# Kernel optimization log

Hardware: AMD Instinct MI355X
Metric: run time of the kernel (lower is better)

Reference implementation:

```python
import jax, jax.numpy as jnp
import numpy as np

B = 8192
L = 2  # number of clipped photonic layers


def _pauli_z_matrix():
    # Z expectation per wire for each of the 16 basis states; wire 0 = MSB.
    k = np.arange(16)
    Z = np.stack([1 - 2 * ((k >> 3) & 1),
                  1 - 2 * ((k >> 2) & 1),
                  1 - 2 * ((k >> 1) & 1),
                  1 - 2 * (k & 1)], axis=1).astype(np.float32)
    return jnp.asarray(Z)  # (16, 4)


def setup_inputs() -> dict:
    key = jax.random.key(0)
    ks = jax.random.split(key, 14)
    x = jax.random.normal(ks[0], (B, 1, 28, 28), dtype=jnp.float32)
    # input photonic layer (no clip)
    w_in = 0.5 * jax.random.normal(ks[1], (2, 2), dtype=jnp.float32)
    b_in = 0.1 * jax.random.normal(ks[2], (2,), dtype=jnp.float32)
    scale_in = 1.0 + 0.1 * jax.random.normal(ks[3], (2,), dtype=jnp.float32)
    shift_in = 0.05 * jax.random.normal(ks[4], (2,), dtype=jnp.float32)
    # L clipped photonic layers (clip applied at construction in torch)
    Wc = jnp.clip(0.5 * jax.random.normal(ks[5], (L, 2, 2), dtype=jnp.float32), -5.0, 5.0)
    bc = jnp.clip(0.1 * jax.random.normal(ks[6], (L, 2), dtype=jnp.float32), -5.0, 5.0)
    scalec = 1.0 + 0.1 * jax.random.normal(ks[7], (L, 2), dtype=jnp.float32)
    shiftc = 0.05 * jax.random.normal(ks[8], (L, 2), dtype=jnp.float32)
    # final linear of classical branch: Linear(2, 1)
    w_out = 0.5 * jax.random.normal(ks[9], (1, 2), dtype=jnp.float32)
    b_out = 0.1 * jax.random.normal(ks[10], (1,), dtype=jnp.float32)
    # fixed random 16x16 unitary standing in for tq.RandomLayer(n_ops=8, 4 wires)
    rng = np.random.default_rng(0)
    A = rng.normal(size=(16, 16)) + 1j * rng.normal(size=(16, 16))
    Q, _ = np.linalg.qr(A)
    U_re = jnp.asarray(Q.real.astype(np.float32))
    U_im = jnp.asarray(Q.imag.astype(np.float32))
    # classifier Linear(785, 1)  (original declares 786 but combined feat is 785)
    w_cls = 0.03 * jax.random.normal(ks[11], (1, 785), dtype=jnp.float32)
    b_cls = 0.1 * jax.random.normal(ks[12], (1,), dtype=jnp.float32)
    return {"x": x, "w_in": w_in, "b_in": b_in, "scale_in": scale_in,
            "shift_in": shift_in, "Wc": Wc, "bc": bc, "scalec": scalec,
            "shiftc": shiftc, "w_out": w_out, "b_out": b_out,
            "U_re": U_re, "U_im": U_im, "w_cls": w_cls, "b_cls": b_cls}


def reference(x, w_in, b_in, scale_in, shift_in, Wc, bc, scalec, shiftc,
              w_out, b_out, U_re, U_im, w_cls, b_cls):
    bsz = x.shape[0]
    # ---- classical branch: mean/std features through photonic-style MLP ----
    mean = jnp.mean(x, axis=(1, 2, 3))[:, None]
    std = jnp.std(x, axis=(1, 2, 3), ddof=1)[:, None]  # torch unbiased std
    h = jnp.concatenate([mean, std], axis=1)  # (B, 2)
    h = jnp.tanh(h @ w_in.T + b_in) * scale_in + shift_in
    for i in range(Wc.shape[0]):
        h = jnp.tanh(h @ Wc[i].T + bc[i]) * scalec[i] + shiftc[i]
    cls_out = h @ w_out.T + b_out  # (B, 1)
    # ---- quantum branch: all 196 2x2 patches batched in one pass ----
    img = x.reshape(bsz, 28, 28)
    # (B,14,2,14,2) -> (B,14,14,2,2) -> (B,196,4) with patch pixel order
    # [x[r,c], x[r,c+1], x[r+1,c], x[r+1,c+1]] matching the torch loop.
    p = img.reshape(bsz, 14, 2, 14, 2).transpose(0, 1, 3, 2, 4).reshape(bsz, 196, 4)
    half = 0.5 * p
    a = jnp.stack([jnp.cos(half), jnp.sin(half)], axis=-1)  # (B,196,4,2) RY|0> amps
    # product state over 4 qubits -> (B,196,16)
    psi = jnp.einsum('bpi,bpj,bpk,bpl->bpijkl',
                     a[:, :, 0], a[:, :, 1], a[:, :, 2], a[:, :, 3]
                     ).reshape(bsz, 196, 16)
    re = psi @ U_re.T
    im = psi @ U_im.T
    probs = re * re + im * im  # (B,196,16)
    Z = _pauli_z_matrix()
    qfeat = (probs @ Z).reshape(bsz, 196 * 4)  # (B, 784)
    # ---- fuse + classify ----
    combined = jnp.concatenate([cls_out, qfeat], axis=1)  # (B, 785)
    logits = combined @ w_cls.T + b_cls
    return jax.nn.sigmoid(logits)
```

## Files before the change

kernel.cpp:

```cpp
#include <hip/hip_runtime.h>
#include <hip/hip_bf16.h>
#include <math.h>


#define NPATCH 196
#define NIMG   8192
#define ROWB   80

typedef __bf16 bf16x8 __attribute__((ext_vector_type(8)));
typedef float  f32x4  __attribute__((ext_vector_type(4)));

union Frag { bf16x8 v; uint4 u; unsigned us[4]; };

static __device__ inline unsigned short bfbits(float f) {
    __hip_bfloat16 h = __float2bfloat16(f);
    unsigned short s; __builtin_memcpy(&s, &h, 2); return s;
}
static __device__ inline unsigned packbf(float lo, float hi) {
    return (unsigned)bfbits(lo) | ((unsigned)bfbits(hi) << 16);
}

__global__ __launch_bounds__(256) void fraud_kernel(
    const float* __restrict__ x,
    const float* __restrict__ w_in,
    const float* __restrict__ b_in,
    const float* __restrict__ scale_in,
    const float* __restrict__ shift_in,
    const float* __restrict__ Wc,
    const float* __restrict__ bc,
    const float* __restrict__ scalec,
    const float* __restrict__ shiftc,
    const float* __restrict__ w_out,
    const float* __restrict__ b_out,
    const float* __restrict__ U_re,
    const float* __restrict__ U_im,
    const float* __restrict__ w_cls,
    const float* __restrict__ b_cls,
    float* __restrict__ out)
{
    __shared__ __align__(16) unsigned char lds[256 * ROWB];
    __shared__ __align__(16) float wlds[784];
    __shared__ float red[3][4];

    const int tid  = threadIdx.x;
    const int lane = tid & 63;
    const int wv   = tid >> 6;
    const int n16  = lane & 15;
    const int q    = lane >> 4;
    const int img  = blockIdx.x;

    for (int i = tid; i < 784; i += 256) wlds[i] = w_cls[1 + i];

    Frag bre, bim;
    bre.u = make_uint4(0u, 0u, 0u, 0u);
    bim.u = make_uint4(0u, 0u, 0u, 0u);
    if (q < 2) {
        const float* pr = U_re + n16 * 16 + q * 8;
        const float* pi = U_im + n16 * 16 + q * 8;
        bre.us[0] = packbf(pr[0], pr[1]); bre.us[1] = packbf(pr[2], pr[3]);
        bre.us[2] = packbf(pr[4], pr[5]); bre.us[3] = packbf(pr[6], pr[7]);
        bim.us[0] = packbf(pi[0], pi[1]); bim.us[1] = packbf(pi[2], pi[3]);
        bim.us[2] = packbf(pi[4], pi[5]); bim.us[3] = packbf(pi[6], pi[7]);
    }

    const float* xp = x + (size_t)img * 784;
    float sum = 0.f, sumsq = 0.f;
    uint4 lo = make_uint4(0u, 0u, 0u, 0u);
    uint4 hi = make_uint4(0u, 0u, 0u, 0u);
    if (tid < NPATCH) {
        const int rr = tid / 14;
        const int cc = tid - rr * 14;
        const float2 top = *(const float2*)(xp + (2 * rr) * 28 + 2 * cc);
        const float2 bot = *(const float2*)(xp + (2 * rr + 1) * 28 + 2 * cc);
        const float x0 = top.x, x1 = top.y, x2 = bot.x, x3 = bot.y;

        sum   = x0 + x1 + x2 + x3;
        sumsq = x0 * x0 + x1 * x1 + x2 * x2 + x3 * x3;

        float s0, c0, s1, c1, s2, c2, s3, c3;
        __sincosf(0.5f * x0, &s0, &c0);
        __sincosf(0.5f * x1, &s1, &c1);
        __sincosf(0.5f * x2, &s2, &c2);
        __sincosf(0.5f * x3, &s3, &c3);

        const float a01[4] = { c0 * c1, c0 * s1, s0 * c1, s0 * s1 };
        const float a23[4] = { c2 * c3, c2 * s3, s2 * c3, s2 * s3 };

        lo.x = packbf(a01[0] * a23[0], a01[0] * a23[1]);
        lo.y = packbf(a01[0] * a23[2], a01[0] * a23[3]);
        lo.z = packbf(a01[1] * a23[0], a01[1] * a23[1]);
        lo.w = packbf(a01[1] * a23[2], a01[1] * a23[3]);
        hi.x = packbf(a01[2] * a23[0], a01[2] * a23[1]);
        hi.y = packbf(a01[2] * a23[2], a01[2] * a23[3]);
        hi.z = packbf(a01[3] * a23[0], a01[3] * a23[1]);
        hi.w = packbf(a01[3] * a23[2], a01[3] * a23[3]);
    }
    unsigned* row = (unsigned*)(lds + tid * ROWB);
    *(uint4*)(row)      = lo;
    *(uint4*)(row + 4)  = hi;
    *(uint4*)(row + 8)  = make_uint4(0u, 0u, 0u, 0u);
    *(uint4*)(row + 12) = make_uint4(0u, 0u, 0u, 0u);
    __syncthreads();

    const float sg0 = (n16 & 8) ? -1.f : 1.f;
    const float sg1 = (n16 & 4) ? -1.f : 1.f;
    const float sg2 = (n16 & 2) ? -1.f : 1.f;
    const float sg3 = (n16 & 1) ? -1.f : 1.f;

    float qacc = 0.f;
    const unsigned char* wb = lds + wv * 64 * ROWB;

    auto do_tile = [&](int t) {
        Frag a;
        a.u = *(const uint4*)(wb + (t * 16 + n16) * ROWB + q * 16);
        f32x4 cr = {0.f, 0.f, 0.f, 0.f}, ci = {0.f, 0.f, 0.f, 0.f};
        cr = __builtin_amdgcn_mfma_f32_16x16x32_bf16(a.v, bre.v, cr, 0, 0, 0);
        ci = __builtin_amdgcn_mfma_f32_16x16x32_bf16(a.v, bim.v, ci, 0, 0, 0);
        #pragma unroll
        for (int j = 0; j < 4; ++j) {
            const int m = wv * 64 + t * 16 + q * 4 + j;
            float zc = 0.f;
            if (m < NPATCH) {
                const float4 wq = *(const float4*)(wlds + 4 * m);
                zc = wq.x * sg0 + wq.y * sg1 + wq.z * sg2 + wq.w * sg3;
            }
            const float prob = cr[j] * cr[j] + ci[j] * ci[j];
            qacc = fmaf(prob, zc, qacc);
        }
    };
    if (wv < 3) {
        do_tile(0); do_tile(1); do_tile(2); do_tile(3);
    } else {
        do_tile(0);
    }

    #pragma unroll
    for (int off = 1; off < 64; off <<= 1) {
        sum   += __shfl_xor(sum,   off, 64);
        sumsq += __shfl_xor(sumsq, off, 64);
        qacc  += __shfl_xor(qacc,  off, 64);
    }
    if (lane == 0) {
        red[0][wv] = sum;
        red[1][wv] = sumsq;
        red[2][wv] = qacc;
    }
    __syncthreads();

    if (tid == 0) {
        const float S  = red[0][0] + red[0][1] + red[0][2] + red[0][3];
        const float SS = red[1][0] + red[1][1] + red[1][2] + red[1][3];
        const float QS = red[2][0] + red[2][1] + red[2][2] + red[2][3];

        const float mean = S * (1.f / 784.f);
        float var = (SS - S * S * (1.f / 784.f)) * (1.f / 783.f);
        var = fmaxf(var, 0.f);
        const float stdv = sqrtf(var);

        float h0 = mean, h1 = stdv;
        {
            const float t0 = tanhf(h0 * w_in[0] + h1 * w_in[1] + b_in[0]);
            const float t1 = tanhf(h0 * w_in[2] + h1 * w_in[3] + b_in[1]);
            h0 = t0 * scale_in[0] + shift_in[0];
            h1 = t1 * scale_in[1] + shift_in[1];
        }
        #pragma unroll
        for (int l = 0; l < 2; ++l) {
            const float t0 = tanhf(h0 * Wc[l * 4 + 0] + h1 * Wc[l * 4 + 1] + bc[l * 2 + 0]);
            const float t1 = tanhf(h0 * Wc[l * 4 + 2] + h1 * Wc[l * 4 + 3] + bc[l * 2 + 1]);
            h0 = t0 * scalec[l * 2 + 0] + shiftc[l * 2 + 0];
            h1 = t1 * scalec[l * 2 + 1] + shiftc[l * 2 + 1];
        }
        const float cls   = h0 * w_out[0] + h1 * w_out[1] + b_out[0];
        const float logit = b_cls[0] + w_cls[0] * cls + QS;
        out[img] = 1.f / (1.f + __expf(-logit));
    }
}

extern "C" void kernel_launch(void* const* d_in, const int* in_sizes, int n_in,
                              void* d_out, int out_size, void* d_ws, size_t ws_size,
                              hipStream_t stream) {
    const float* x        = (const float*)d_in[0];
    const float* w_in     = (const float*)d_in[1];
    const float* b_in     = (const float*)d_in[2];
    const float* scale_in = (const float*)d_in[3];
    const float* shift_in = (const float*)d_in[4];
    const float* Wc       = (const float*)d_in[5];
    const float* bc       = (const float*)d_in[6];
    const float* scalec   = (const float*)d_in[7];
    const float* shiftc   = (const float*)d_in[8];
    const float* w_out    = (const float*)d_in[9];
    const float* b_out    = (const float*)d_in[10];
    const float* U_re     = (const float*)d_in[11];
    const float* U_im     = (const float*)d_in[12];
    const float* w_cls    = (const float*)d_in[13];
    const float* b_cls    = (const float*)d_in[14];
    float* out = (float*)d_out;

    fraud_kernel<<<NIMG, 256, 0, stream>>>(x, w_in, b_in, scale_in, shift_in,
                                           Wc, bc, scalec, shiftc, w_out, b_out,
                                           U_re, U_im, w_cls, b_cls, out);
}
```

Baseline: 115.7 us.

## Process 16 images per block with per-wave image loop and precomputed Z weights

```diff
diff --git a/kernel.cpp b/kernel.cpp
--- a/kernel.cpp
+++ b/kernel.cpp
@@ -5,6 +5,8 @@
 
 #define NPATCH 196
 #define NIMG   8192
+#define GIMG   16
+#define NBLK   (NIMG / GIMG)
 #define ROWB   80
 
 typedef __bf16 bf16x8 __attribute__((ext_vector_type(8)));
@@ -18,6 +20,25 @@
 }
 static __device__ inline unsigned packbf(float lo, float hi) {
     return (unsigned)bfbits(lo) | ((unsigned)bfbits(hi) << 16);
+}
+
+static __device__ inline void psi_pack(float x0, float x1, float x2, float x3,
+                                       uint4& lo, uint4& hi) {
+    float s0, c0, s1, c1, s2, c2, s3, c3;
+    __sincosf(0.5f * x0, &s0, &c0);
+    __sincosf(0.5f * x1, &s1, &c1);
+    __sincosf(0.5f * x2, &s2, &c2);
+    __sincosf(0.5f * x3, &s3, &c3);
+    const float a01[4] = { c0 * c1, c0 * s1, s0 * c1, s0 * s1 };
+    const float a23[4] = { c2 * c3, c2 * s3, s2 * c3, s2 * s3 };
+    lo.x = packbf(a01[0] * a23[0], a01[0] * a23[1]);
+    lo.y = packbf(a01[0] * a23[2], a01[0] * a23[3]);
+    lo.z = packbf(a01[1] * a23[0], a01[1] * a23[1]);
+    lo.w = packbf(a01[1] * a23[2], a01[1] * a23[3]);
+    hi.x = packbf(a01[2] * a23[0], a01[2] * a23[1]);
+    hi.y = packbf(a01[2] * a23[2], a01[2] * a23[3]);
+    hi.z = packbf(a01[3] * a23[0], a01[3] * a23[1]);
+    hi.w = packbf(a01[3] * a23[2], a01[3] * a23[3]);
 }
 
 __global__ __launch_bounds__(256) void fraud_kernel(
@@ -39,17 +60,23 @@
     float* __restrict__ out)
 {
     __shared__ __align__(16) unsigned char lds[256 * ROWB];
-    __shared__ __align__(16) float wlds[784];
-    __shared__ float red[3][4];
+    __shared__ float zc[NPATCH * 17];
+    __shared__ float accS[GIMG], accV[GIMG], accQ[GIMG];
 
     const int tid  = threadIdx.x;
     const int lane = tid & 63;
     const int wv   = tid >> 6;
     const int n16  = lane & 15;
     const int q    = lane >> 4;
-    const int img  = blockIdx.x;
-
-    for (int i = tid; i < 784; i += 256) wlds[i] = w_cls[1 + i];
+    const int img0 = blockIdx.x * GIMG;
+
+    for (int i = tid; i < NPATCH * 16; i += 256) {
+        const int m = i >> 4, n = i & 15;
+        const float* wp = w_cls + 1 + 4 * m;
+        const float w0 = wp[0], w1 = wp[1], w2 = wp[2], w3 = wp[3];
+        zc[m * 17 + n] = ((n & 8) ? -w0 : w0) + ((n & 4) ? -w1 : w1)
+                       + ((n & 2) ? -w2 : w2) + ((n & 1) ? -w3 : w3);
+    }
 
     Frag bre, bim;
     bre.u = make_uint4(0u, 0u, 0u, 0u);
@@ -63,94 +90,130 @@
         bim.us[2] = packbf(pi[4], pi[5]); bim.us[3] = packbf(pi[6], pi[7]);
     }
 
-    const float* xp = x + (size_t)img * 784;
-    float sum = 0.f, sumsq = 0.f;
-    uint4 lo = make_uint4(0u, 0u, 0u, 0u);
-    uint4 hi = make_uint4(0u, 0u, 0u, 0u);
-    if (tid < NPATCH) {
-        const int rr = tid / 14;
-        const int cc = tid - rr * 14;
+    unsigned char* wbase = lds + wv * 64 * ROWB;
+    unsigned* myrow = (unsigned*)(wbase + lane * ROWB);
+    *(uint4*)(myrow + 8)  = make_uint4(0u, 0u, 0u, 0u);
+    *(uint4*)(myrow + 12) = make_uint4(0u, 0u, 0u, 0u);
+
+    __syncthreads();
+
+    const int imgw0 = img0 + wv * 4;
+
+    float2 ctop, cbot;
+    {
+        const int p = lane, rr = p / 14, cc = p - rr * 14;
+        const float* xp = x + (size_t)imgw0 * 784;
+        ctop = *(const float2*)(xp + (2 * rr) * 28 + 2 * cc);
+        cbot = *(const float2*)(xp + (2 * rr + 1) * 28 + 2 * cc);
+    }
+
+    float rS = 0.f, rV = 0.f, rQ = 0.f;
+
+    #pragma unroll 3
+    for (int idx = 0; idx < 12; ++idx) {
+        const int im = idx / 3;
+        const int c  = idx - im * 3;
+        const float x0 = ctop.x, x1 = ctop.y, x2 = cbot.x, x3 = cbot.y;
+
+        if (idx < 11) {
+            const int nidx = idx + 1;
+            const int nim = nidx / 3, nc = nidx - nim * 3;
+            const int p = nc * 64 + lane, rr = p / 14, cc = p - rr * 14;
+            const float* xp = x + (size_t)(imgw0 + nim) * 784;
+            ctop = *(const float2*)(xp + (2 * rr) * 28 + 2 * cc);
+            cbot = *(const float2*)(xp + (2 * rr + 1) * 28 + 2 * cc);
+        }
+
+        rS += x0 + x1 + x2 + x3;
+        rV += x0 * x0 + x1 * x1 + x2 * x2 + x3 * x3;
+
+        uint4 lo, hi;
+        psi_pack(x0, x1, x2, x3, lo, hi);
+        *(uint4*)(myrow)     = lo;
+        *(uint4*)(myrow + 4) = hi;
+        asm volatile("s_waitcnt lgkmcnt(0)" ::: "memory");
+
+        #pragma unroll
+        for (int t = 0; t < 4; ++t) {
+            Frag a;
+            a.u = *(const uint4*)(wbase + (t * 16 + n16) * ROWB + q * 16);
+            f32x4 cr = {0.f, 0.f, 0.f, 0.f}, ci = {0.f, 0.f, 0.f, 0.f};
+            cr = __builtin_amdgcn_mfma_f32_16x16x32_bf16(a.v, bre.v, cr, 0, 0, 0);
+            ci = __builtin_amdgcn_mfma_f32_16x16x32_bf16(a.v, bim.v, ci, 0, 0, 0);
+            const int pb = (c * 64 + t * 16 + q * 4) * 17 + n16;
+            #pragma unroll
+            for (int j = 0; j < 4; ++j) {
+                const float prob = cr[j] * cr[j] + ci[j] * ci[j];
+                rQ = fmaf(prob, zc[pb + 17 * j], rQ);
+            }
+        }
+
+        if (c == 2) {
+            #pragma unroll
+            for (int off = 1; off < 64; off <<= 1) {
+                rS += __shfl_xor(rS, off, 64);
+                rV += __shfl_xor(rV, off, 64);
+                rQ += __shfl_xor(rQ, off, 64);
+            }
+            if (lane == 0) {
+                accS[wv * 4 + im] = rS;
+                accV[wv * 4 + im] = rV;
+                accQ[wv * 4 + im] = rQ;
+            }
+            rS = 0.f; rV = 0.f; rQ = 0.f;
+        }
+    }
+
+    float tS = 0.f, tV = 0.f;
+    if (lane < 16) {
+        const int iml = lane >> 2;
+        const int p   = 192 + (lane & 3);
+        const int rr = p / 14, cc = p - rr * 14;
+        const float* xp = x + (size_t)(imgw0 + iml) * 784;
         const float2 top = *(const float2*)(xp + (2 * rr) * 28 + 2 * cc);
         const float2 bot = *(const float2*)(xp + (2 * rr + 1) * 28 + 2 * cc);
         const float x0 = top.x, x1 = top.y, x2 = bot.x, x3 = bot.y;
-
-        sum   = x0 + x1 + x2 + x3;
-        sumsq = x0 * x0 + x1 * x1 + x2 * x2 + x3 * x3;
-
-        float s0, c0, s1, c1, s2, c2, s3, c3;
-        __sincosf(0.5f * x0, &s0, &c0);
-        __sincosf(0.5f * x1, &s1, &c1);
-        __sincosf(0.5f * x2, &s2, &c2);
-        __sincosf(0.5f * x3, &s3, &c3);
-
-        const float a01[4] = { c0 * c1, c0 * s1, s0 * c1, s0 * s1 };
-        const float a23[4] = { c2 * c3, c2 * s3, s2 * c3, s2 * s3 };
-
-        lo.x = packbf(a01[0] * a23[0], a01[0] * a23[1]);
-        lo.y = packbf(a01[0] * a23[2], a01[0] * a23[3]);
-        lo.z = packbf(a01[1] * a23[0], a01[1] * a23[1]);
-        lo.w = packbf(a01[1] * a23[2], a01[1] * a23[3]);
-        hi.x = packbf(a01[2] * a23[0], a01[2] * a23[1]);
-        hi.y = packbf(a01[2] * a23[2], a01[2] * a23[3]);
-        hi.z = packbf(a01[3] * a23[0], a01[3] * a23[1]);
-        hi.w = packbf(a01[3] * a23[2], a01[3] * a23[3]);
-    }
-    unsigned* row = (unsigned*)(lds + tid * ROWB);
-    *(uint4*)(row)      = lo;
-    *(uint4*)(row + 4)  = hi;
-    *(uint4*)(row + 8)  = make_uint4(0u, 0u, 0u, 0u);
-    *(uint4*)(row + 12) = make_uint4(0u, 0u, 0u, 0u);
-    __syncthreads();
-
-    const float sg0 = (n16 & 8) ? -1.f : 1.f;
-    const float sg1 = (n16 & 4) ? -1.f : 1.f;
-    const float sg2 = (n16 & 2) ? -1.f : 1.f;
-    const float sg3 = (n16 & 1) ? -1.f : 1.f;
-
-    float qacc = 0.f;
-    const unsigned char* wb = lds + wv * 64 * ROWB;
-
-    auto do_tile = [&](int t) {
+        tS = x0 + x1 + x2 + x3;
+        tV = x0 * x0 + x1 * x1 + x2 * x2 + x3 * x3;
+        uint4 lo, hi;
+        psi_pack(x0, x1, x2, x3, lo, hi);
+        *(uint4*)(myrow)     = lo;
+        *(uint4*)(myrow + 4) = hi;
+    }
+    asm volatile("s_waitcnt lgkmcnt(0)" ::: "memory");
+
+    float tQ = 0.f;
+    {
         Frag a;
-        a.u = *(const uint4*)(wb + (t * 16 + n16) * ROWB + q * 16);
+        a.u = *(const uint4*)(wbase + n16 * ROWB + q * 16);
         f32x4 cr = {0.f, 0.f, 0.f, 0.f}, ci = {0.f, 0.f, 0.f, 0.f};
         cr = __builtin_amdgcn_mfma_f32_16x16x32_bf16(a.v, bre.v, cr, 0, 0, 0);
         ci = __builtin_amdgcn_mfma_f32_16x16x32_bf16(a.v, bim.v, ci, 0, 0, 0);
         #pragma unroll
         for (int j = 0; j < 4; ++j) {
-            const int m = wv * 64 + t * 16 + q * 4 + j;
-            float zc = 0.f;
-            if (m < NPATCH) {
-                const float4 wq = *(const float4*)(wlds + 4 * m);
-                zc = wq.x * sg0 + wq.y * sg1 + wq.z * sg2 + wq.w * sg3;
-            }
             const float prob = cr[j] * cr[j] + ci[j] * ci[j];
-            qacc = fmaf(prob, zc, qacc);
-        }
-    };
-    if (wv < 3) {
-        do_tile(0); do_tile(1); do_tile(2); do_tile(3);
-    } else {
-        do_tile(0);
-    }
-
-    #pragma unroll
-    for (int off = 1; off < 64; off <<= 1) {
-        sum   += __shfl_xor(sum,   off, 64);
-        sumsq += __shfl_xor(sumsq, off, 64);
-        qacc  += __shfl_xor(qacc,  off, 64);
-    }
-    if (lane == 0) {
-        red[0][wv] = sum;
-        red[1][wv] = sumsq;
-        red[2][wv] = qacc;
+            tQ = fmaf(prob, zc[(192 + j) * 17 + n16], tQ);
+        }
+    }
+    tS += __shfl_xor(tS, 1, 64);  tS += __shfl_xor(tS, 2, 64);
+    tV += __shfl_xor(tV, 1, 64);  tV += __shfl_xor(tV, 2, 64);
+    tQ += __shfl_xor(tQ, 1, 64);  tQ += __shfl_xor(tQ, 2, 64);
+    tQ += __shfl_xor(tQ, 4, 64);  tQ += __shfl_xor(tQ, 8, 64);
+
+    if (lane < 16 && (lane & 3) == 0) {
+        const int iml = lane >> 2;
+        accS[wv * 4 + iml] += tS;
+        accV[wv * 4 + iml] += tV;
+    }
+    if (n16 == 0) {
+        accQ[wv * 4 + q] += tQ;
     }
     __syncthreads();
 
-    if (tid == 0) {
-        const float S  = red[0][0] + red[0][1] + red[0][2] + red[0][3];
-        const float SS = red[1][0] + red[1][1] + red[1][2] + red[1][3];
-        const float QS = red[2][0] + red[2][1] + red[2][2] + red[2][3];
+    if (tid < GIMG) {
+        const float S  = accS[tid];
+        const float SS = accV[tid];
+        const float QS = accQ[tid];
 
         const float mean = S * (1.f / 784.f);
         float var = (SS - S * S * (1.f / 784.f)) * (1.f / 783.f);
@@ -173,7 +236,7 @@
         }
         const float cls   = h0 * w_out[0] + h1 * w_out[1] + b_out[0];
         const float logit = b_cls[0] + w_cls[0] * cls + QS;
-        out[img] = 1.f / (1.f + __expf(-logit));
+        out[img0 + tid] = 1.f / (1.f + __expf(-logit));
     }
 }
 
@@ -197,7 +260,7 @@
     const float* b_cls    = (const float*)d_in[14];
     float* out = (float*)d_out;
 
-    fraud_kernel<<<NIMG, 256, 0, stream>>>(x, w_in, b_in, scale_in, shift_in,
+    fraud_kernel<<<NBLK, 256, 0, stream>>>(x, w_in, b_in, scale_in, shift_in,
                                            Wc, bc, scalec, shiftc, w_out, b_out,
                                            U_re, U_im, w_cls, b_cls, out);
 }
```

Result: faster. 109.2 us, median of 2 (-5.7%).
